# Performance work log

Hardware: AMD Instinct MI355X
Metric: run time of the kernel (lower is better)

The kernel has to match this reference:

```python
import jax, jax.numpy as jnp
import numpy as np

B, T, D, H, R = 4, 4096, 1024, 16, 256
DH = D // H  # 64


def setup_inputs() -> dict:
    key = jax.random.key(0)
    ks = jax.random.split(key, 5)
    s = 0.02
    return {
        "x": jax.random.normal(ks[0], (B, T, D), dtype=jnp.float32),
        "Wq": jax.random.normal(ks[1], (D, D), dtype=jnp.float32) * s,
        "bq": jnp.zeros((D,), dtype=jnp.float32),
        "Wd": jax.random.normal(ks[2], (D, R), dtype=jnp.float32) * s,
        "bd": jnp.zeros((R,), dtype=jnp.float32),
        "Wu": jax.random.normal(ks[3], (R, 2 * D), dtype=jnp.float32) * s,
        "bu": jnp.zeros((2 * D,), dtype=jnp.float32),
        "Wo": jax.random.normal(ks[4], (D, D), dtype=jnp.float32) * s,
        "bo": jnp.zeros((D,), dtype=jnp.float32),
    }


def reference(x, Wq, bq, Wd, bd, Wu, bu, Wo, bo):
    b, t = x.shape[0], x.shape[1]
    # q projection -> (B,T,H,DH)
    q = (x @ Wq + bq).reshape(b, t, H, DH)
    # low-rank KV: down then up -> (B,T,H,2*DH)
    kv = ((x @ Wd + bd) @ Wu + bu).reshape(b, t, H, 2 * DH)
    k, v = kv[..., :DH], kv[..., DH:]
    # elu+1 feature map
    q = jax.nn.elu(q) + 1.0
    k = jax.nn.elu(k) + 1.0
    # linear attention: context = k^T v per head -> (B,H,DH,DH)
    context = jnp.einsum("bthd,bthe->bhde", k, v)
    out = jnp.einsum("bthd,bhde->bthe", q, context)  # (B,T,H,DH)
    # normalizer: q . sum_t(k)
    k_sum = k.sum(axis=1)  # (B,H,DH)
    z = 1.0 / (jnp.einsum("bthd,bhd->bth", q, k_sum) + 1e-6)
    out = out * z[..., None]
    return out.reshape(b, t, D) @ Wo + bo
```

## Files before the change

### kernel.cpp

```cpp
#include <hip/hip_runtime.h>
#include <hip/hip_bf16.h>
#include <cstddef>
#include <cstdint>

#define B_  4
#define T_  4096
#define D_  1024
#define H_  16
#define DH_ 64
#define R_  256
#define BT_ (B_ * T_)
#define TWO_D_ (2 * D_)

typedef __attribute__((ext_vector_type(8))) short short8;
typedef __attribute__((ext_vector_type(4))) float f32x4;

__device__ __forceinline__ float elu1(float x) {
    return x > 0.0f ? x + 1.0f : __expf(x);
}

__device__ __forceinline__ float bf2f(short u) {
    union { uint32_t i; float f; } c;
    c.i = ((uint32_t)(uint16_t)u) << 16;
    return c.f;
}

typedef __attribute__((address_space(1))) void void_g;
typedef __attribute__((address_space(3))) void void_l;
__device__ __forceinline__ void gld_lds16(const void* g, void* l) {
    __builtin_amdgcn_global_load_lds(
        (const void_g*)(uintptr_t)g,
        (void_l*)(uint32_t)(uintptr_t)l,
        16, 0, 0);
}

#define BM 128
#define BN 128
#define BK 32

__device__ __forceinline__ void store_out(float* p, float v) { *p = v; }
__device__ __forceinline__ void store_out(__hip_bfloat16* p, float v) { *p = __float2bfloat16(v); }

template<int EPI, bool BROW, typename OT>
__global__ __launch_bounds__(256) void gemm_bf16(
    const __hip_bfloat16* __restrict__ A,
    const __hip_bfloat16* __restrict__ Bt,
    const float* __restrict__ bias,
    OT* __restrict__ C,
    OT* __restrict__ C2,
    int M, int N, int K)
{
    __shared__ alignas(16) __hip_bfloat16 As[BM * BK];
    __shared__ alignas(16) __hip_bfloat16 Bs[BN * BK];

    const int nbx = N / BN;
    const int id = blockIdx.x;
    const int strip = id / (8 * nbx);
    const int wi = id % (8 * nbx);
    const int bm = (strip * 8 + (wi & 7)) * BM;
    const int bn = (wi >> 3) * BN;

    const int tid  = threadIdx.x;
    const int lane = tid & 63;
    const int wm   = (tid >> 7) * 64;
    const int wn   = ((tid >> 6) & 1) * 64;
    const int r15  = lane & 15;
    const int kg   = lane >> 4;

    f32x4 acc[4][4] = {};

    const int c0 = tid, c1 = tid + 256;
    const __hip_bfloat16* a0 = A  + (size_t)(bm + (c0 >> 2)) * K + (c0 & 3) * 8;
    const __hip_bfloat16* a1 = A  + (size_t)(bm + (c1 >> 2)) * K + (c1 & 3) * 8;
    const __hip_bfloat16* b0 = Bt + (size_t)(bn + (c0 >> 2)) * K + (c0 & 3) * 8;
    const __hip_bfloat16* b1 = Bt + (size_t)(bn + (c1 >> 2)) * K + (c1 & 3) * 8;

    for (int k0 = 0; k0 < K; k0 += BK) {
        gld_lds16(a0 + k0, As + c0 * 8);
        gld_lds16(a1 + k0, As + c1 * 8);
        gld_lds16(b0 + k0, Bs + c0 * 8);
        gld_lds16(b1 + k0, Bs + c1 * 8);
        __syncthreads();

        short8 af[4], bf[4];
#pragma unroll
        for (int i = 0; i < 4; ++i) {
            af[i] = *(const short8*)(As + (wm + i * 16 + r15) * BK + kg * 8);
            bf[i] = *(const short8*)(Bs + (wn + i * 16 + r15) * BK + kg * 8);
        }
#pragma unroll
        for (int i = 0; i < 4; ++i)
#pragma unroll
            for (int j = 0; j < 4; ++j)
                acc[i][j] = __builtin_amdgcn_mfma_f32_16x16x32_bf16(af[i], bf[j], acc[i][j], 0, 0, 0);
        __syncthreads();
    }

    const int row0 = bm + wm + (lane >> 4) * 4;

    if (EPI == 3) {
        const bool qreg = (bn < 1024);
#pragma unroll
        for (int j = 0; j < 4; ++j) {
            const int col = bn + wn + j * 16 + r15;
            const float bv = bias[col];
#pragma unroll
            for (int i = 0; i < 4; ++i)
#pragma unroll
                for (int r = 0; r < 4; ++r) {
                    const int row = row0 + i * 16 + r;
                    float v = acc[i][j][r] + bv;
                    if (qreg) {
                        store_out(C + (size_t)row * 1024 + col, elu1(v));
                    } else {
                        store_out(C2 + (size_t)row * 256 + (col - 1024), v);
                    }
                }
        }
        return;
    }

    float brow[4][4];
    if (BROW) {
#pragma unroll
        for (int i = 0; i < 4; ++i)
#pragma unroll
            for (int r = 0; r < 4; ++r) brow[i][r] = bias[row0 + i * 16 + r];
    }
#pragma unroll
    for (int j = 0; j < 4; ++j) {
        const int col = bn + wn + j * 16 + r15;
        const float bv = BROW ? 0.0f : bias[col];
        const bool kp_col = ((col & 127) < 64);
#pragma unroll
        for (int i = 0; i < 4; ++i) {
#pragma unroll
            for (int r = 0; r < 4; ++r) {
                const int row = row0 + i * 16 + r;
                float v = acc[i][j][r] + (BROW ? brow[i][r] : bv);
                if (EPI == 1) v = elu1(v);
                else if (EPI == 2) {
                    const bool kp = BROW ? ((row & 127) < 64) : kp_col;
                    if (kp) v = elu1(v);
                }
                store_out(C + (size_t)row * N + col, v);
            }
        }
    }
}

__global__ __launch_bounds__(256) void cast_bf16_kernel(
    const float* __restrict__ s, __hip_bfloat16* __restrict__ d, int n)
{
    const int i = (blockIdx.x * 256 + threadIdx.x) * 8;
    if (i >= n) return;
    float4 v0 = *(const float4*)(s + i);
    float4 v1 = *(const float4*)(s + i + 4);
    __hip_bfloat16 t[8];
    t[0] = __float2bfloat16(v0.x); t[1] = __float2bfloat16(v0.y);
    t[2] = __float2bfloat16(v0.z); t[3] = __float2bfloat16(v0.w);
    t[4] = __float2bfloat16(v1.x); t[5] = __float2bfloat16(v1.y);
    t[6] = __float2bfloat16(v1.z); t[7] = __float2bfloat16(v1.w);
    *(short8*)(d + i) = *(const short8*)t;
}

__global__ __launch_bounds__(256) void transpose_cast(
    const float* __restrict__ W, __hip_bfloat16* __restrict__ Wt, int K, int N)
{
    __shared__ float t[32][33];
    const int n0 = blockIdx.x * 32, k0 = blockIdx.y * 32;
    const int c = threadIdx.x & 31, r = threadIdx.x >> 5;
#pragma unroll
    for (int rr = r; rr < 32; rr += 8)
        t[rr][c] = W[(size_t)(k0 + rr) * N + n0 + c];
    __syncthreads();
#pragma unroll
    for (int rr = r; rr < 32; rr += 8)
        Wt[(size_t)(n0 + rr) * K + k0 + c] = __float2bfloat16(t[c][rr]);
}

__global__ __launch_bounds__(256) void concat_bias(
    const float* __restrict__ bq, const float* __restrict__ bd,
    float* __restrict__ o)
{
    const int i = blockIdx.x * 256 + threadIdx.x;
    o[i] = (i < 1024) ? bq[i] : bd[i - 1024];
}

#define CHT 512

__global__ __launch_bounds__(256) void ctx_mfma(
    const __hip_bfloat16* __restrict__ kvT, float* __restrict__ ctx,
    float* __restrict__ ksum)
{
    __shared__ alignas(16) unsigned char smem[40960];
    float* red0 = (float*)smem;
    float* red1 = (float*)(smem + 20480);

    const int bh = blockIdx.x >> 3;
    const int chunk = blockIdx.x & 7;
    const int b = bh >> 4;
    const int h = bh & 15;
    const int tid = threadIdx.x;
    const int lane = tid & 63;
    const int w = tid >> 6;
    const int r15 = lane & 15;
    const int kg  = lane >> 4;

    f32x4 acc[4][4] = {};
    f32x4 acc4[4] = {};

    const short one = (short)0x3F80;
    const short8 bfv = (r15 == 0)
        ? (short8){one, one, one, one, one, one, one, one}
        : (short8){0, 0, 0, 0, 0, 0, 0, 0};

    const size_t tbase = (size_t)b * T_ + (size_t)chunk * CHT;
    const __hip_bfloat16* src = kvT + (size_t)(h * 128) * BT_ + tbase;

    for (int it = 0; it < CHT / 128; ++it) {
#pragma unroll
        for (int r = 0; r < 8; ++r) {
            const int c = r * 256 + tid;
            const int s = c >> 9, j = (c >> 2) & 127, u = c & 3;
            gld_lds16(src + (size_t)j * BT_ + it * 128 + s * 32 + u * 8,
                      smem + c * 16);
        }
        __syncthreads();

        const __hip_bfloat16* Ls = (const __hip_bfloat16*)smem;
        short8 af[4], bf[4];
#pragma unroll
        for (int i = 0; i < 4; ++i) {
            af[i] = *(const short8*)(Ls + (w * 128 + i * 16 + r15) * 32 + kg * 8);
            bf[i] = *(const short8*)(Ls + (w * 128 + 64 + i * 16 + r15) * 32 + kg * 8);
        }
#pragma unroll
        for (int i = 0; i < 4; ++i) {
#pragma unroll
            for (int j = 0; j < 4; ++j)
                acc[i][j] = __builtin_amdgcn_mfma_f32_16x16x32_bf16(af[i], bf[j], acc[i][j], 0, 0, 0);
            acc4[i] = __builtin_amdgcn_mfma_f32_16x16x32_bf16(af[i], bfv, acc4[i], 0, 0, 0);
        }
        __syncthreads();
    }

    const int q4 = lane >> 4;
    auto wr = [&](float* reg) {
#pragma unroll
        for (int i = 0; i < 4; ++i) {
#pragma unroll
            for (int r = 0; r < 4; ++r) {
                const int row = i * 16 + q4 * 4 + r;
#pragma unroll
                for (int j = 0; j < 4; ++j) reg[row * 80 + j * 16 + r15] = acc[i][j][r];
                reg[row * 80 + 64 + r15] = acc4[i][r];
            }
        }
    };
    auto rd = [&](const float* reg) {
#pragma unroll
        for (int i = 0; i < 4; ++i) {
#pragma unroll
            for (int r = 0; r < 4; ++r) {
                const int row = i * 16 + q4 * 4 + r;
#pragma unroll
                for (int j = 0; j < 4; ++j) acc[i][j][r] += reg[row * 80 + j * 16 + r15];
                acc4[i][r] += reg[row * 80 + 64 + r15];
            }
        }
    };

    if (w == 1) wr(red0);
    if (w == 3) wr(red1);
    __syncthreads();
    if (w == 0) rd(red0);
    if (w == 2) rd(red1);
    __syncthreads();
    if (w == 2) wr(red0);
    __syncthreads();
    if (w == 0) { rd(red0); wr(red0); }
    __syncthreads();

    float* cdst = ctx + (size_t)bh * 4096;
#pragma unroll
    for (int r = 0; r < 16; ++r) {
        const int idx = r * 256 + tid;
        const int d = idx >> 6, e = idx & 63;
        atomicAdd(cdst + idx, red0[d * 80 + e]);
    }
    if (tid < 64) atomicAdd(ksum + bh * 64 + tid, red0[tid * 80 + 64]);
}

__global__ __launch_bounds__(256) void pack_ctx(
    const float* __restrict__ ctx, __hip_bfloat16* __restrict__ ctxT)
{
    __shared__ float L[64 * 65];
    const int bh = blockIdx.x;
    const int tid = threadIdx.x;
#pragma unroll
    for (int r = 0; r < 16; ++r) {
        const int idx = r * 256 + tid;
        L[(idx >> 6) * 65 + (idx & 63)] = ctx[(size_t)bh * 4096 + idx];
    }
    __syncthreads();
#pragma unroll
    for (int r = 0; r < 16; ++r) {
        const int idx = r * 256 + tid;
        ctxT[(size_t)bh * 4096 + idx] =
            __float2bfloat16(L[(idx & 63) * 65 + (idx >> 6)]);
    }
}

__global__ __launch_bounds__(256) void out_mfma(
    const __hip_bfloat16* __restrict__ qb, const __hip_bfloat16* __restrict__ ctxT,
    const float* __restrict__ ksum, __hip_bfloat16* __restrict__ outb)
{
    __shared__ alignas(16) unsigned char As[256 * 128];
    __shared__ alignas(16) unsigned char Bs[64 * 128];
    __shared__ float ksumL[64];
    __shared__ float zbuf[256];

    const int bh = blockIdx.x >> 4;
    const int tile = blockIdx.x & 15;
    const int b = bh >> 4;
    const int h = bh & 15;
    const int tid = threadIdx.x;
    const int lane = tid & 63;
    const int w = tid >> 6;
    const int r15 = lane & 15;
    const int kg  = lane >> 4;

    const size_t trow0 = (size_t)b * T_ + (size_t)tile * 256;

#pragma unroll
    for (int r = 0; r < 8; ++r) {
        const int c = r * 256 + tid;
        const int row = c >> 3, slot = c & 7, u = slot ^ (row & 7);
        gld_lds16(qb + (trow0 + row) * D_ + h * 64 + u * 8, As + c * 16);
    }
#pragma unroll
    for (int r = 0; r < 2; ++r) {
        const int c = r * 256 + tid;
        const int row = c >> 3, slot = c & 7, u = slot ^ (row & 7);
        gld_lds16(ctxT + (size_t)bh * 4096 + row * 64 + u * 8, Bs + c * 16);
    }
    if (tid < 64) ksumL[tid] = ksum[bh * 64 + tid];
    __syncthreads();

    short8 af[4][2], bf[4][2];
#pragma unroll
    for (int i = 0; i < 4; ++i)
#pragma unroll
        for (int s = 0; s < 2; ++s) {
            const int m = w * 64 + i * 16 + r15;
            const int n = i * 16 + r15;
            const int uk = s * 4 + kg;
            af[i][s] = *(const short8*)(As + m * 128 + ((uk ^ (m & 7)) * 16));
            bf[i][s] = *(const short8*)(Bs + n * 128 + ((uk ^ (n & 7)) * 16));
        }

    f32x4 acc[4][4] = {};
#pragma unroll
    for (int s = 0; s < 2; ++s)
#pragma unroll
        for (int i = 0; i < 4; ++i)
#pragma unroll
            for (int j = 0; j < 4; ++j)
                acc[i][j] = __builtin_amdgcn_mfma_f32_16x16x32_bf16(af[i][s], bf[j][s], acc[i][j], 0, 0, 0);

    float dsum[4];
#pragma unroll
    for (int i = 0; i < 4; ++i) {
        float s0 = 0.0f;
#pragma unroll
        for (int s = 0; s < 2; ++s)
#pragma unroll
            for (int j8 = 0; j8 < 8; ++j8)
                s0 += bf2f(af[i][s][j8]) * ksumL[s * 32 + kg * 8 + j8];
        s0 += __shfl_xor(s0, 16);
        s0 += __shfl_xor(s0, 32);
        dsum[i] = s0;
    }
    if (lane < 16) {
#pragma unroll
        for (int i = 0; i < 4; ++i)
            zbuf[w * 64 + i * 16 + lane] = 1.0f / (dsum[i] + 1e-6f);
    }
    __syncthreads();

    const int q4 = lane >> 4;
#pragma unroll
    for (int i = 0; i < 4; ++i) {
#pragma unroll
        for (int r = 0; r < 4; ++r) {
            const int m = w * 64 + i * 16 + q4 * 4 + r;
            const float z = zbuf[m];
#pragma unroll
            for (int j = 0; j < 4; ++j) {
                outb[(trow0 + m) * D_ + h * 64 + j * 16 + r15] =
                    __float2bfloat16(acc[i][j][r] * z);
            }
        }
    }
}

extern "C" void kernel_launch(void* const* d_in, const int* in_sizes, int n_in,
                              void* d_out, int out_size, void* d_ws, size_t ws_size,
                              hipStream_t stream) {
    const float* x  = (const float*)d_in[0];
    const float* Wq = (const float*)d_in[1];
    const float* bq = (const float*)d_in[2];
    const float* Wd = (const float*)d_in[3];
    const float* bd = (const float*)d_in[4];
    const float* Wu = (const float*)d_in[5];
    const float* bu = (const float*)d_in[6];
    const float* Wo = (const float*)d_in[7];
    const float* bo = (const float*)d_in[8];
    float* out = (float*)d_out;

    __hip_bfloat16* xb    = (__hip_bfloat16*)d_ws;
    __hip_bfloat16* WqdT  = xb    + (size_t)BT_ * D_;
    __hip_bfloat16* WuT   = WqdT  + (size_t)1280 * D_;
    __hip_bfloat16* WoT   = WuT   + (size_t)TWO_D_ * R_;
    __hip_bfloat16* xdb   = WoT   + (size_t)D_ * D_;
    __hip_bfloat16* kvT   = xdb   + (size_t)BT_ * R_;
    __hip_bfloat16* qb    = kvT   + (size_t)TWO_D_ * BT_;
    float* bias_qd = (float*)(qb + (size_t)BT_ * D_);
    float* ctx  = bias_qd + 1280;
    float* ksum = ctx + (size_t)B_ * H_ * DH_ * DH_;
    __hip_bfloat16* ctxT = (__hip_bfloat16*)(ksum + B_ * H_ * DH_);
    __hip_bfloat16* outb = xb;

    hipMemsetAsync(ctx, 0,
        (size_t)(B_ * H_ * DH_ * DH_ + B_ * H_ * DH_) * sizeof(float), stream);

    cast_bf16_kernel<<<(BT_ * D_) / (8 * 256), 256, 0, stream>>>(x, xb, BT_ * D_);
    transpose_cast<<<dim3(D_ / 32, D_ / 32), 256, 0, stream>>>(Wq, WqdT, D_, D_);
    transpose_cast<<<dim3(R_ / 32, D_ / 32), 256, 0, stream>>>(Wd, WqdT + (size_t)D_ * D_, D_, R_);
    transpose_cast<<<dim3(TWO_D_ / 32, R_ / 32), 256, 0, stream>>>(Wu, WuT, R_, TWO_D_);
    transpose_cast<<<dim3(D_ / 32, D_ / 32), 256, 0, stream>>>(Wo, WoT, D_, D_);
    concat_bias<<<5, 256, 0, stream>>>(bq, bd, bias_qd);

    gemm_bf16<3, false, __hip_bfloat16><<<(BT_ / BM) * (1280 / BN), 256, 0, stream>>>(
        xb, WqdT, bias_qd, qb, xdb, BT_, 1280, D_);
    gemm_bf16<2, true, __hip_bfloat16><<<(TWO_D_ / BM) * (BT_ / BN), 256, 0, stream>>>(
        WuT, xdb, bu, kvT, nullptr, TWO_D_, BT_, R_);
    ctx_mfma<<<64 * (T_ / CHT), 256, 0, stream>>>(kvT, ctx, ksum);
    pack_ctx<<<64, 256, 0, stream>>>(ctx, ctxT);
    out_mfma<<<64 * 16, 256, 0, stream>>>(qb, ctxT, ksum, outb);
    gemm_bf16<0, false, float><<<(BT_ / BM) * (D_ / BN), 256, 0, stream>>>(
        outb, WoT, bo, out, nullptr, BT_, D_, D_);
}
```

Baseline: 354.0 us.

## Switch GEMM to 32x32x16 MFMA with XOR-swizzled LDS layout

```diff
diff --git a/kernel.cpp b/kernel.cpp
--- a/kernel.cpp
+++ b/kernel.cpp
@@ -14,6 +14,7 @@
 
 typedef __attribute__((ext_vector_type(8))) short short8;
 typedef __attribute__((ext_vector_type(4))) float f32x4;
+typedef __attribute__((ext_vector_type(16))) float f32x16;
 
 __device__ __forceinline__ float elu1(float x) {
     return x > 0.0f ? x + 1.0f : __expf(x);
@@ -64,16 +65,18 @@
     const int lane = tid & 63;
     const int wm   = (tid >> 7) * 64;
     const int wn   = ((tid >> 6) & 1) * 64;
-    const int r15  = lane & 15;
-    const int kg   = lane >> 4;
-
-    f32x4 acc[4][4] = {};
+    const int l31  = lane & 31;
+    const int hi   = lane >> 5;
+
+    f32x16 acc[2][2] = {};
 
     const int c0 = tid, c1 = tid + 256;
-    const __hip_bfloat16* a0 = A  + (size_t)(bm + (c0 >> 2)) * K + (c0 & 3) * 8;
-    const __hip_bfloat16* a1 = A  + (size_t)(bm + (c1 >> 2)) * K + (c1 & 3) * 8;
-    const __hip_bfloat16* b0 = Bt + (size_t)(bn + (c0 >> 2)) * K + (c0 & 3) * 8;
-    const __hip_bfloat16* b1 = Bt + (size_t)(bn + (c1 >> 2)) * K + (c1 & 3) * 8;
+    const int u0 = (c0 & 3) ^ ((c0 >> 3) & 3);
+    const int u1 = (c1 & 3) ^ ((c1 >> 3) & 3);
+    const __hip_bfloat16* a0 = A  + (size_t)(bm + (c0 >> 2)) * K + u0 * 8;
+    const __hip_bfloat16* a1 = A  + (size_t)(bm + (c1 >> 2)) * K + u1 * 8;
+    const __hip_bfloat16* b0 = Bt + (size_t)(bn + (c0 >> 2)) * K + u0 * 8;
+    const __hip_bfloat16* b1 = Bt + (size_t)(bn + (c1 >> 2)) * K + u1 * 8;
 
     for (int k0 = 0; k0 < K; k0 += BK) {
         gld_lds16(a0 + k0, As + c0 * 8);
@@ -82,61 +85,67 @@
         gld_lds16(b1 + k0, Bs + c1 * 8);
         __syncthreads();
 
-        short8 af[4], bf[4];
-#pragma unroll
-        for (int i = 0; i < 4; ++i) {
-            af[i] = *(const short8*)(As + (wm + i * 16 + r15) * BK + kg * 8);
-            bf[i] = *(const short8*)(Bs + (wn + i * 16 + r15) * BK + kg * 8);
-        }
-#pragma unroll
-        for (int i = 0; i < 4; ++i)
-#pragma unroll
-            for (int j = 0; j < 4; ++j)
-                acc[i][j] = __builtin_amdgcn_mfma_f32_16x16x32_bf16(af[i], bf[j], acc[i][j], 0, 0, 0);
+        short8 af[2][2], bf[2][2];
+#pragma unroll
+        for (int i = 0; i < 2; ++i)
+#pragma unroll
+            for (int s = 0; s < 2; ++s) {
+                const int ca = s * 2 + hi;
+                const int ra = wm + i * 32 + l31;
+                af[i][s] = *(const short8*)(As + ra * 32 + (ca ^ ((ra >> 1) & 3)) * 8);
+                const int rb = wn + i * 32 + l31;
+                bf[i][s] = *(const short8*)(Bs + rb * 32 + (ca ^ ((rb >> 1) & 3)) * 8);
+            }
+#pragma unroll
+        for (int s = 0; s < 2; ++s)
+#pragma unroll
+            for (int i = 0; i < 2; ++i)
+#pragma unroll
+                for (int j = 0; j < 2; ++j)
+                    acc[i][j] = __builtin_amdgcn_mfma_f32_32x32x16_bf16(
+                        af[i][s], bf[j][s], acc[i][j], 0, 0, 0);
         __syncthreads();
     }
 
-    const int row0 = bm + wm + (lane >> 4) * 4;
+    const int rbase = bm + wm + 4 * hi;
 
     if (EPI == 3) {
         const bool qreg = (bn < 1024);
 #pragma unroll
-        for (int j = 0; j < 4; ++j) {
-            const int col = bn + wn + j * 16 + r15;
+        for (int j = 0; j < 2; ++j) {
+            const int col = bn + wn + j * 32 + l31;
             const float bv = bias[col];
 #pragma unroll
-            for (int i = 0; i < 4; ++i)
-#pragma unroll
-                for (int r = 0; r < 4; ++r) {
-                    const int row = row0 + i * 16 + r;
+            for (int i = 0; i < 2; ++i)
+#pragma unroll
+                for (int r = 0; r < 16; ++r) {
+                    const int row = rbase + i * 32 + (r & 3) + 8 * (r >> 2);
                     float v = acc[i][j][r] + bv;
-                    if (qreg) {
-                        store_out(C + (size_t)row * 1024 + col, elu1(v));
-                    } else {
-                        store_out(C2 + (size_t)row * 256 + (col - 1024), v);
-                    }
+                    if (qreg) store_out(C + (size_t)row * 1024 + col, elu1(v));
+                    else      store_out(C2 + (size_t)row * 256 + (col - 1024), v);
                 }
         }
         return;
     }
 
-    float brow[4][4];
+    float brow[2][16];
     if (BROW) {
 #pragma unroll
-        for (int i = 0; i < 4; ++i)
-#pragma unroll
-            for (int r = 0; r < 4; ++r) brow[i][r] = bias[row0 + i * 16 + r];
-    }
-#pragma unroll
-    for (int j = 0; j < 4; ++j) {
-        const int col = bn + wn + j * 16 + r15;
+        for (int i = 0; i < 2; ++i)
+#pragma unroll
+            for (int r = 0; r < 16; ++r)
+                brow[i][r] = bias[rbase + i * 32 + (r & 3) + 8 * (r >> 2)];
+    }
+#pragma unroll
+    for (int j = 0; j < 2; ++j) {
+        const int col = bn + wn + j * 32 + l31;
         const float bv = BROW ? 0.0f : bias[col];
         const bool kp_col = ((col & 127) < 64);
 #pragma unroll
-        for (int i = 0; i < 4; ++i) {
-#pragma unroll
-            for (int r = 0; r < 4; ++r) {
-                const int row = row0 + i * 16 + r;
+        for (int i = 0; i < 2; ++i) {
+#pragma unroll
+            for (int r = 0; r < 16; ++r) {
+                const int row = rbase + i * 32 + (r & 3) + 8 * (r >> 2);
                 float v = acc[i][j][r] + (BROW ? brow[i][r] : bv);
                 if (EPI == 1) v = elu1(v);
                 else if (EPI == 2) {
```

Measured after the change: 354.9 us. Within noise of the previous version (+0.2%).
